# Optimization experiments

Hardware: AMD Instinct MI355X
Metric: run time of the kernel (lower is better)

Reference implementation:

```python
import jax, jax.numpy as jnp
import numpy as np

N = 100000

def _gcn_conv(x, W, b, row, col, norm, n_nodes):
    # x: [N, Fin], W: [Fin, Fout]; message = norm * (x W)[row], aggregated at col
    h = x @ W                                  # small GEMM
    msg = h[row] * norm[:, None]               # [E+N, Fout] gather (memory bound)
    out = jax.ops.segment_sum(msg, col, num_segments=n_nodes)
    return out + b

def _norm_coeffs(edge_index, n_nodes):
    # add self-loops, compute symmetric normalization deg^-1/2[row]*deg^-1/2[col]
    loops = jnp.arange(n_nodes, dtype=edge_index.dtype)
    row = jnp.concatenate([edge_index[0], loops])
    col = jnp.concatenate([edge_index[1], loops])
    deg = jax.ops.segment_sum(jnp.ones_like(col, dtype=jnp.float32), col,
                              num_segments=n_nodes)
    dinv = jnp.where(deg > 0, jax.lax.rsqrt(deg), 0.0)
    norm = dinv[row] * dinv[col]
    return row, col, norm

def setup_inputs() -> dict:
    key = jax.random.key(0)
    ks = jax.random.split(key, 4)
    x = jax.random.normal(ks[0], (N, 64), dtype=jnp.float32)
    edge_index = jax.random.randint(ks[1], (2, 1600000), 0, N, dtype=jnp.int64)
    W1 = jax.random.normal(ks[2], (64, 64), dtype=jnp.float32) / np.sqrt(64)
    b1 = jnp.zeros((64,), dtype=jnp.float32)
    W2 = jax.random.normal(ks[3], (64, 64), dtype=jnp.float32) / np.sqrt(64)
    b2 = jnp.zeros((64,), dtype=jnp.float32)
    return {"x": x, "edge_index": edge_index, "W1": W1, "b1": b1, "W2": W2, "b2": b2}

def reference(x, edge_index, W1, b1, W2, b2):
    row, col, norm = _norm_coeffs(edge_index, N)
    h = jax.nn.relu(_gcn_conv(x, W1, b1, row, col, norm, N))
    return _gcn_conv(h, W2, b2, row, col, norm, N)
```

## Files before the change

### kernel.cpp

```cpp
#include <hip/hip_runtime.h>


#define NPB 32
#define BSH 8
#define BSZ 256
#define PTILE 4096
#define CAP 6144
#define PADALLOW 3856
#define CROW (CAP + PADALLOW)

typedef __attribute__((ext_vector_type(8))) short bf16x8;
typedef __attribute__((ext_vector_type(4))) float f32x4;

__device__ __forceinline__ unsigned bf16_rne(float f) {
    unsigned b = __float_as_uint(f);
    return (b + 0x7fffu + ((b >> 16) & 1u)) >> 16;
}
__device__ __forceinline__ float bf16_lo(unsigned u) { return __uint_as_float(u << 16); }
__device__ __forceinline__ float bf16_hi(unsigned u) { return __uint_as_float(u & 0xffff0000u); }

__global__ __launch_bounds__(512) void k_count(const int* __restrict__ coli,
                                               int E, int N, int NB, int numTiles,
                                               int* __restrict__ tcnt) {
    __shared__ int hist[512];
    int t = threadIdx.x;
    int T = E + N;
    int tile = blockIdx.x;
    int tstart = tile * PTILE;
    int m = min(PTILE, T - tstart);
    for (int b = t; b < NB; b += 512) hist[b] = 0;
    __syncthreads();
    for (int i = t; i < m; i += 512) {
        int g = tstart + i;
        int c = (g < E) ? coli[g] : (g - E);
        atomicAdd(&hist[c >> BSH], 1);
    }
    __syncthreads();
    for (int b = t; b < NB; b += 512) tcnt[(size_t)tile * NB + b] = hist[b];
}

__global__ __launch_bounds__(512) void k_scan(int* __restrict__ tcnt,
                                              int* __restrict__ btot,
                                              int NB, int numTiles) {
    __shared__ int wsum[8];
    int b = blockIdx.x;
    int t = threadIdx.x;
    int lane = t & 63, wid = t >> 6;
    int base = 0;
    for (int c0 = 0; c0 < numTiles; c0 += 512) {
        int tt = c0 + t;
        int v = (tt < numTiles) ? tcnt[(size_t)tt * NB + b] : 0;
        int inc = v;
        #pragma unroll
        for (int d = 1; d < 64; d <<= 1) {
            int o = __shfl_up(inc, d);
            if (lane >= d) inc += o;
        }
        if (lane == 63) wsum[wid] = inc;
        __syncthreads();
        int woff = 0, ctot = 0;
        #pragma unroll
        for (int i = 0; i < 8; i++) {
            int s = wsum[i];
            if (i < wid) woff += s;
            ctot += s;
        }
        if (tt < numTiles) tcnt[(size_t)tt * NB + b] = b * CAP + base + woff + inc - v;
        base += ctot;
        __syncthreads();
    }
    if (t == 0) btot[b] = base;
}

__global__ __launch_bounds__(512) void k_scatter(const int* __restrict__ rowi,
                                                 const int* __restrict__ coli,
                                                 int E, int N, int NB, int numTiles,
                                                 const int* __restrict__ tcnt,
                                                 unsigned* __restrict__ pairs) {
    __shared__ int hist[512];
    __shared__ int lbase[512];
    __shared__ int gbase[512];
    __shared__ unsigned sorted[PTILE];
    __shared__ unsigned short sbkt[PTILE];
    __shared__ int wsum[8];
    int t = threadIdx.x;
    int T = E + N;
    int tile = blockIdx.x;
    int tstart = tile * PTILE;
    int m = min(PTILE, T - tstart);
    for (int b = t; b < NB; b += 512) {
        hist[b] = 0;
        gbase[b] = tcnt[(size_t)tile * NB + b];
    }
    __syncthreads();
    int c_reg[8];
    #pragma unroll
    for (int k = 0; k < 8; k++) {
        int i = t + k * 512;
        int c = 0;
        if (i < m) {
            int g = tstart + i;
            c = (g < E) ? coli[g] : (g - E);
            atomicAdd(&hist[c >> BSH], 1);
        }
        c_reg[k] = c;
    }
    __syncthreads();
    {
        int lane = t & 63, wid = t >> 6;
        int v = (t < NB) ? hist[t] : 0;
        int inc = v;
        #pragma unroll
        for (int d = 1; d < 64; d <<= 1) {
            int o = __shfl_up(inc, d);
            if (lane >= d) inc += o;
        }
        if (lane == 63) wsum[wid] = inc;
        __syncthreads();
        int woff = 0;
        for (int i = 0; i < wid; i++) woff += wsum[i];
        if (t < NB) lbase[t] = woff + inc - v;
        __syncthreads();
    }
    for (int b = t; b < NB; b += 512) hist[b] = 0;
    __syncthreads();
    #pragma unroll
    for (int k = 0; k < 8; k++) {
        int i = t + k * 512;
        if (i < m) {
            int g = tstart + i;
            int c = c_reg[k];
            int r = (g < E) ? rowi[g] : c;
            int b = c >> BSH;
            int lr = atomicAdd(&hist[b], 1);
            int pos = lbase[b] + lr;
            sorted[pos] = (unsigned)r | ((unsigned)(c & (BSZ - 1)) << 24);
            sbkt[pos] = (unsigned short)b;
        }
    }
    __syncthreads();
    for (int j = t; j < m; j += 512) {
        int b = sbkt[j];
        pairs[gbase[b] + (j - lbase[b])] = sorted[j];
    }
}

__global__ __launch_bounds__(1024) void k_bfill(const unsigned* __restrict__ pairs,
                                                const int* __restrict__ btot,
                                                int N,
                                                int* __restrict__ offsets,
                                                int* __restrict__ cnt,
                                                float* __restrict__ dinv,
                                                int* __restrict__ csrc) {
    __shared__ int scnt[BSZ];
    __shared__ int scur[BSZ];
    __shared__ int wsum[4];
    __shared__ int scsrc[CROW];
    int b = blockIdx.x;
    int t = threadIdx.x;
    int ebeg = b * CAP;
    int m = btot[b];
    int pbase = b * CROW;
    if (t < BSZ) scnt[t] = 0;
    __syncthreads();
    for (int i = t; i < m; i += 1024) {
        atomicAdd(&scnt[pairs[ebeg + i] >> 24], 1);
    }
    __syncthreads();
    int cval = 0, pc = 0, inc = 0;
    int lane = t & 63, wid = t >> 6;
    if (t < BSZ) {
        cval = scnt[t];
        pc = (cval + 15) & ~15;
        inc = pc;
        #pragma unroll
        for (int d = 1; d < 64; d <<= 1) {
            int o = __shfl_up(inc, d);
            if (lane >= d) inc += o;
        }
        if (lane == 63) wsum[wid] = inc;
    }
    __syncthreads();
    if (t < BSZ) {
        int woff = 0;
        for (int i = 0; i < wid; i++) woff += wsum[i];
        int offl = woff + inc - pc;
        int v = (b << BSH) + t;
        if (v < N) {
            offsets[v] = pbase + offl;
            cnt[v] = (cval + 1) & ~1;
            dinv[v] = rsqrtf((float)cval);
        }
        scur[t] = offl;
        for (int i = offl + cval; i < offl + pc; i++) scsrc[i] = N;
    }
    __syncthreads();
    for (int i = t; i < m; i += 1024) {
        unsigned pk = pairs[ebeg + i];
        int slot = atomicAdd(&scur[pk >> 24], 1);
        scsrc[slot] = (int)(pk & 0xFFFFFFu);
    }
    __syncthreads();
    int tot = wsum[0] + wsum[1] + wsum[2] + wsum[3];
    for (int j = t; j < tot; j += 1024) csrc[pbase + j] = scsrc[j];
}

template <bool BF16IN>
__global__ __launch_bounds__(256) void k_gemm(const void* __restrict__ Xv,
                                              const float* __restrict__ W,
                                              const float* __restrict__ dinv,
                                              unsigned* __restrict__ Hout,
                                              int N, int nSlabs, int slabStride) {
    __shared__ float SMEM[4224];
    int t = threadIdx.x;
    int lane = t & 63, w = t >> 6;
    int nn = lane & 15, kq = lane >> 4;

    for (int i = t; i < 1024; i += 256) ((float4*)SMEM)[i] = ((const float4*)W)[i];
    __syncthreads();
    bf16x8 Bf[2][4];
    #pragma unroll
    for (int kt = 0; kt < 2; kt++) {
        #pragma unroll
        for (int ct = 0; ct < 4; ct++) {
            union { bf16x8 v; unsigned short s[8]; } u;
            #pragma unroll
            for (int j = 0; j < 8; j++) {
                int k = kt * 32 + kq * 8 + j;
                u.s[j] = (unsigned short)bf16_rne(SMEM[k * 64 + ct * 16 + nn]);
            }
            Bf[kt][ct] = u.v;
        }
    }
    __syncthreads();

    float* outT = SMEM + w * 1056;

    for (int slab = blockIdx.x * 4 + w; slab < nSlabs; slab += slabStride) {
        int row0 = slab * 16;
        int rowA = min(row0 + nn, N - 1);
        bf16x8 A0, A1;
        if (BF16IN) {
            const uint4* X = (const uint4*)Xv;
            union { uint4 u; bf16x8 v; } a0, a1;
            a0.u = X[(size_t)rowA * 8 + kq];
            a1.u = X[(size_t)rowA * 8 + 4 + kq];
            A0 = a0.v; A1 = a1.v;
        } else {
            const float4* X = (const float4*)Xv;
            float4 f0 = X[(size_t)rowA * 16 + kq * 2];
            float4 f1 = X[(size_t)rowA * 16 + kq * 2 + 1];
            float4 f2 = X[(size_t)rowA * 16 + 8 + kq * 2];
            float4 f3 = X[(size_t)rowA * 16 + 8 + kq * 2 + 1];
            union { bf16x8 v; unsigned short s[8]; } a0, a1;
            a0.s[0] = (unsigned short)bf16_rne(f0.x); a0.s[1] = (unsigned short)bf16_rne(f0.y);
            a0.s[2] = (unsigned short)bf16_rne(f0.z); a0.s[3] = (unsigned short)bf16_rne(f0.w);
            a0.s[4] = (unsigned short)bf16_rne(f1.x); a0.s[5] = (unsigned short)bf16_rne(f1.y);
            a0.s[6] = (unsigned short)bf16_rne(f1.z); a0.s[7] = (unsigned short)bf16_rne(f1.w);
            a1.s[0] = (unsigned short)bf16_rne(f2.x); a1.s[1] = (unsigned short)bf16_rne(f2.y);
            a1.s[2] = (unsigned short)bf16_rne(f2.z); a1.s[3] = (unsigned short)bf16_rne(f2.w);
            a1.s[4] = (unsigned short)bf16_rne(f3.x); a1.s[5] = (unsigned short)bf16_rne(f3.y);
            a1.s[6] = (unsigned short)bf16_rne(f3.z); a1.s[7] = (unsigned short)bf16_rne(f3.w);
            A0 = a0.v; A1 = a1.v;
        }
        float dvm = dinv[rowA];

        f32x4 acc[4];
        #pragma unroll
        for (int ct = 0; ct < 4; ct++) acc[ct] = (f32x4){0.f, 0.f, 0.f, 0.f};
        #pragma unroll
        for (int ct = 0; ct < 4; ct++) {
            acc[ct] = __builtin_amdgcn_mfma_f32_16x16x32_bf16(A0, Bf[0][ct], acc[ct], 0, 0, 0);
            acc[ct] = __builtin_amdgcn_mfma_f32_16x16x32_bf16(A1, Bf[1][ct], acc[ct], 0, 0, 0);
        }

        #pragma unroll
        for (int reg = 0; reg < 4; reg++) {
            int r = kq * 4 + reg;
            float dv = __shfl(dvm, r);
            #pragma unroll
            for (int ct = 0; ct < 4; ct++) {
                outT[r * 66 + ct * 16 + nn] = acc[ct][reg] * dv;
            }
        }
        int rr = lane >> 2;
        int c0 = (lane & 3) * 16;
        int orow = row0 + rr;
        if (orow < N) {
            unsigned pk[8];
            #pragma unroll
            for (int i = 0; i < 8; i++) {
                float lo = outT[rr * 66 + c0 + 2 * i];
                float hi = outT[rr * 66 + c0 + 2 * i + 1];
                pk[i] = bf16_rne(lo) | (bf16_rne(hi) << 16);
            }
            uint4* dst = (uint4*)Hout + (size_t)orow * 8 + (lane & 3) * 2;
            dst[0] = make_uint4(pk[0], pk[1], pk[2], pk[3]);
            dst[1] = make_uint4(pk[4], pk[5], pk[6], pk[7]);
        } else if (orow == N) {
            uint4* dst = (uint4*)Hout + (size_t)N * 8 + (lane & 3) * 2;
            dst[0] = make_uint4(0, 0, 0, 0);
            dst[1] = make_uint4(0, 0, 0, 0);
        }
    }
}

template <bool RELU_BF16OUT>
__global__ __launch_bounds__(256) void k_agg(const uint4* __restrict__ H,
                                             const int* __restrict__ offsets,
                                             const int* __restrict__ cnt,
                                             const int* __restrict__ csrc,
                                             const float* __restrict__ dinv,
                                             const float* __restrict__ bias,
                                             void* __restrict__ outv, int N) {
    int t = threadIdx.x;
    int fl = t & 7;
    int v = blockIdx.x * NPB + (t >> 3);
    if (v >= N) return;
    int beg = offsets[v];
    int deg = cnt[v];
    const int2* cs2 = (const int2*)(csrc + beg);
    const char* hb = (const char*)H + ((unsigned)fl << 4);

    float a0 = 0.f, a1 = 0.f, a2 = 0.f, a3 = 0.f;
    float a4 = 0.f, a5 = 0.f, a6 = 0.f, a7 = 0.f;

#define ACC8(R) do {                                                        \
        uint4 dd = *(const uint4*)(hb + ((unsigned)(R) << 7));              \
        a0 += bf16_lo(dd.x); a1 += bf16_hi(dd.x);                           \
        a2 += bf16_lo(dd.y); a3 += bf16_hi(dd.y);                           \
        a4 += bf16_lo(dd.z); a5 += bf16_hi(dd.z);                           \
        a6 += bf16_lo(dd.w); a7 += bf16_hi(dd.w);                           \
    } while (0)

    int2 ss = cs2[0];
    for (int j = 2; j < deg; j += 2) {
        int2 nx = cs2[j >> 1];
        ACC8(ss.x);
        ACC8(ss.y);
        ss = nx;
    }
    ACC8(ss.x);
    ACC8(ss.y);
#undef ACC8

    float dv = dinv[v];
    const float4* b4 = (const float4*)bias;
    float4 bA = b4[fl * 2];
    float4 bB = b4[fl * 2 + 1];
    float r0 = fmaf(dv, a0, bA.x);
    float r1 = fmaf(dv, a1, bA.y);
    float r2 = fmaf(dv, a2, bA.z);
    float r3 = fmaf(dv, a3, bA.w);
    float r4 = fmaf(dv, a4, bB.x);
    float r5 = fmaf(dv, a5, bB.y);
    float r6 = fmaf(dv, a6, bB.z);
    float r7 = fmaf(dv, a7, bB.w);
    if (RELU_BF16OUT) {
        r0 = fmaxf(r0, 0.f); r1 = fmaxf(r1, 0.f);
        r2 = fmaxf(r2, 0.f); r3 = fmaxf(r3, 0.f);
        r4 = fmaxf(r4, 0.f); r5 = fmaxf(r5, 0.f);
        r6 = fmaxf(r6, 0.f); r7 = fmaxf(r7, 0.f);
        uint4 pk;
        pk.x = bf16_rne(r0) | (bf16_rne(r1) << 16);
        pk.y = bf16_rne(r2) | (bf16_rne(r3) << 16);
        pk.z = bf16_rne(r4) | (bf16_rne(r5) << 16);
        pk.w = bf16_rne(r6) | (bf16_rne(r7) << 16);
        ((uint4*)outv)[(size_t)v * 8 + fl] = pk;
    } else {
        float4* o = (float4*)outv + (size_t)v * 16 + fl * 2;
        o[0] = make_float4(r0, r1, r2, r3);
        o[1] = make_float4(r4, r5, r6, r7);
    }
}

extern "C" void kernel_launch(void* const* d_in, const int* in_sizes, int n_in,
                              void* d_out, int out_size, void* d_ws, size_t ws_size,
                              hipStream_t stream) {
    const float* x  = (const float*)d_in[0];
    const int*   ei = (const int*)d_in[1];
    const float* W1 = (const float*)d_in[2];
    const float* b1 = (const float*)d_in[3];
    const float* W2 = (const float*)d_in[4];
    const float* b2 = (const float*)d_in[5];
    float* out      = (float*)d_out;

    const int N = in_sizes[0] / 64;
    const int E = in_sizes[1] / 2;
    const int* row = ei;
    const int* col = ei + E;
    const int T = E + N;
    const int NB = (N + BSZ - 1) >> BSH;
    const int numTiles = (T + PTILE - 1) / PTILE;

    char* p = (char*)d_ws;
    auto alloc = [&](size_t bytes) { void* r = (void*)p; p += (bytes + 255) & ~(size_t)255; return r; };
    int*      tcnt    = (int*)alloc((size_t)NB * numTiles * 4);
    int*      btot    = (int*)alloc((size_t)(NB + 1) * 4);
    int*      offsets = (int*)alloc((size_t)N * 4);
    int*      cnt     = (int*)alloc((size_t)N * 4);
    float*    dinv    = (float*)alloc((size_t)N * 4);
    unsigned* pairs   = (unsigned*)alloc((size_t)NB * CAP * 4);
    int*      csrc    = (int*)alloc(((size_t)NB * CROW + 64) * 4);
    unsigned* hbuf    = (unsigned*)alloc((size_t)(N + 16) * 32 * 4);
    unsigned* abuf    = (unsigned*)alloc((size_t)(N + 16) * 32 * 4);

    k_count<<<numTiles, 512, 0, stream>>>(col, E, N, NB, numTiles, tcnt);
    k_scan<<<NB, 512, 0, stream>>>(tcnt, btot, NB, numTiles);
    k_scatter<<<numTiles, 512, 0, stream>>>(row, col, E, N, NB, numTiles, tcnt, pairs);
    k_bfill<<<NB, 1024, 0, stream>>>(pairs, btot, N, offsets, cnt, dinv, csrc);

    const int nSlabs = (N + 16) / 16;
    const int GEMM_BLOCKS = 1024;
    const int SLAB_STRIDE = GEMM_BLOCKS * 4;
    const int GB = (N + NPB - 1) / NPB;

    k_gemm<false><<<GEMM_BLOCKS, 256, 0, stream>>>(x, W1, dinv, hbuf, N, nSlabs, SLAB_STRIDE);
    k_agg<true><<<GB, 256, 0, stream>>>((const uint4*)hbuf, offsets, cnt, csrc, dinv, b1, abuf, N);
    k_gemm<true><<<GEMM_BLOCKS, 256, 0, stream>>>(abuf, W2, dinv, hbuf, N, nSlabs, SLAB_STRIDE);
    k_agg<false><<<GB, 256, 0, stream>>>((const uint4*)hbuf, offsets, cnt, csrc, dinv, b2, out, N);
}
```

Baseline: 198.0 us.

## Fuse scatter with first GEMM and merge tail stages behind grid barriers

```diff
diff --git a/kernel.cpp b/kernel.cpp
--- a/kernel.cpp
+++ b/kernel.cpp
@@ -1,13 +1,14 @@
 #include <hip/hip_runtime.h>
 
 
-#define NPB 32
 #define BSH 8
 #define BSZ 256
 #define PTILE 4096
 #define CAP 6144
 #define PADALLOW 3856
 #define CROW (CAP + PADALLOW)
+#define GEMMB 1024
+#define TGRID 768
 
 typedef __attribute__((ext_vector_type(8))) short bf16x8;
 typedef __attribute__((ext_vector_type(4))) float f32x4;
@@ -19,9 +20,21 @@
 __device__ __forceinline__ float bf16_lo(unsigned u) { return __uint_as_float(u << 16); }
 __device__ __forceinline__ float bf16_hi(unsigned u) { return __uint_as_float(u & 0xffff0000u); }
 
+__device__ __forceinline__ void gbar(int* bar, int idx, int nblk) {
+    __syncthreads();
+    if (threadIdx.x == 0) {
+        __threadfence();
+        __hip_atomic_fetch_add(&bar[idx], 1, __ATOMIC_ACQ_REL, __HIP_MEMORY_SCOPE_AGENT);
+        while (__hip_atomic_load(&bar[idx], __ATOMIC_ACQUIRE, __HIP_MEMORY_SCOPE_AGENT) < nblk)
+            __builtin_amdgcn_s_sleep(1);
+    }
+    __syncthreads();
+}
+
 __global__ __launch_bounds__(512) void k_count(const int* __restrict__ coli,
                                                int E, int N, int NB, int numTiles,
-                                               int* __restrict__ tcnt) {
+                                               int* __restrict__ tcnt,
+                                               int* __restrict__ deg) {
     __shared__ int hist[512];
     int t = threadIdx.x;
     int T = E + N;
@@ -34,9 +47,10 @@
         int g = tstart + i;
         int c = (g < E) ? coli[g] : (g - E);
         atomicAdd(&hist[c >> BSH], 1);
-    }
-    __syncthreads();
-    for (int b = t; b < NB; b += 512) tcnt[(size_t)tile * NB + b] = hist[b];
+        atomicAdd(&deg[c], 1);
+    }
+    __syncthreads();
+    for (int b = t; b < NB; b += 512) tcnt[tile * NB + b] = hist[b];
 }
 
 __global__ __launch_bounds__(512) void k_scan(int* __restrict__ tcnt,
@@ -49,7 +63,7 @@
     int base = 0;
     for (int c0 = 0; c0 < numTiles; c0 += 512) {
         int tt = c0 + t;
-        int v = (tt < numTiles) ? tcnt[(size_t)tt * NB + b] : 0;
+        int v = (tt < numTiles) ? tcnt[tt * NB + b] : 0;
         int inc = v;
         #pragma unroll
         for (int d = 1; d < 64; d <<= 1) {
@@ -65,158 +79,26 @@
             if (i < wid) woff += s;
             ctot += s;
         }
-        if (tt < numTiles) tcnt[(size_t)tt * NB + b] = b * CAP + base + woff + inc - v;
+        if (tt < numTiles) tcnt[tt * NB + b] = b * CAP + base + woff + inc - v;
         base += ctot;
         __syncthreads();
     }
     if (t == 0) btot[b] = base;
 }
 
-__global__ __launch_bounds__(512) void k_scatter(const int* __restrict__ rowi,
-                                                 const int* __restrict__ coli,
-                                                 int E, int N, int NB, int numTiles,
-                                                 const int* __restrict__ tcnt,
-                                                 unsigned* __restrict__ pairs) {
-    __shared__ int hist[512];
-    __shared__ int lbase[512];
-    __shared__ int gbase[512];
-    __shared__ unsigned sorted[PTILE];
-    __shared__ unsigned short sbkt[PTILE];
-    __shared__ int wsum[8];
-    int t = threadIdx.x;
-    int T = E + N;
-    int tile = blockIdx.x;
-    int tstart = tile * PTILE;
-    int m = min(PTILE, T - tstart);
-    for (int b = t; b < NB; b += 512) {
-        hist[b] = 0;
-        gbase[b] = tcnt[(size_t)tile * NB + b];
-    }
-    __syncthreads();
-    int c_reg[8];
-    #pragma unroll
-    for (int k = 0; k < 8; k++) {
-        int i = t + k * 512;
-        int c = 0;
-        if (i < m) {
-            int g = tstart + i;
-            c = (g < E) ? coli[g] : (g - E);
-            atomicAdd(&hist[c >> BSH], 1);
-        }
-        c_reg[k] = c;
-    }
-    __syncthreads();
-    {
-        int lane = t & 63, wid = t >> 6;
-        int v = (t < NB) ? hist[t] : 0;
-        int inc = v;
-        #pragma unroll
-        for (int d = 1; d < 64; d <<= 1) {
-            int o = __shfl_up(inc, d);
-            if (lane >= d) inc += o;
-        }
-        if (lane == 63) wsum[wid] = inc;
-        __syncthreads();
-        int woff = 0;
-        for (int i = 0; i < wid; i++) woff += wsum[i];
-        if (t < NB) lbase[t] = woff + inc - v;
-        __syncthreads();
-    }
-    for (int b = t; b < NB; b += 512) hist[b] = 0;
-    __syncthreads();
-    #pragma unroll
-    for (int k = 0; k < 8; k++) {
-        int i = t + k * 512;
-        if (i < m) {
-            int g = tstart + i;
-            int c = c_reg[k];
-            int r = (g < E) ? rowi[g] : c;
-            int b = c >> BSH;
-            int lr = atomicAdd(&hist[b], 1);
-            int pos = lbase[b] + lr;
-            sorted[pos] = (unsigned)r | ((unsigned)(c & (BSZ - 1)) << 24);
-            sbkt[pos] = (unsigned short)b;
-        }
-    }
-    __syncthreads();
-    for (int j = t; j < m; j += 512) {
-        int b = sbkt[j];
-        pairs[gbase[b] + (j - lbase[b])] = sorted[j];
-    }
-}
-
-__global__ __launch_bounds__(1024) void k_bfill(const unsigned* __restrict__ pairs,
-                                                const int* __restrict__ btot,
-                                                int N,
-                                                int* __restrict__ offsets,
-                                                int* __restrict__ cnt,
-                                                float* __restrict__ dinv,
-                                                int* __restrict__ csrc) {
-    __shared__ int scnt[BSZ];
-    __shared__ int scur[BSZ];
-    __shared__ int wsum[4];
-    __shared__ int scsrc[CROW];
-    int b = blockIdx.x;
-    int t = threadIdx.x;
-    int ebeg = b * CAP;
-    int m = btot[b];
-    int pbase = b * CROW;
-    if (t < BSZ) scnt[t] = 0;
-    __syncthreads();
-    for (int i = t; i < m; i += 1024) {
-        atomicAdd(&scnt[pairs[ebeg + i] >> 24], 1);
-    }
-    __syncthreads();
-    int cval = 0, pc = 0, inc = 0;
-    int lane = t & 63, wid = t >> 6;
-    if (t < BSZ) {
-        cval = scnt[t];
-        pc = (cval + 15) & ~15;
-        inc = pc;
-        #pragma unroll
-        for (int d = 1; d < 64; d <<= 1) {
-            int o = __shfl_up(inc, d);
-            if (lane >= d) inc += o;
-        }
-        if (lane == 63) wsum[wid] = inc;
-    }
-    __syncthreads();
-    if (t < BSZ) {
-        int woff = 0;
-        for (int i = 0; i < wid; i++) woff += wsum[i];
-        int offl = woff + inc - pc;
-        int v = (b << BSH) + t;
-        if (v < N) {
-            offsets[v] = pbase + offl;
-            cnt[v] = (cval + 1) & ~1;
-            dinv[v] = rsqrtf((float)cval);
-        }
-        scur[t] = offl;
-        for (int i = offl + cval; i < offl + pc; i++) scsrc[i] = N;
-    }
-    __syncthreads();
-    for (int i = t; i < m; i += 1024) {
-        unsigned pk = pairs[ebeg + i];
-        int slot = atomicAdd(&scur[pk >> 24], 1);
-        scsrc[slot] = (int)(pk & 0xFFFFFFu);
-    }
-    __syncthreads();
-    int tot = wsum[0] + wsum[1] + wsum[2] + wsum[3];
-    for (int j = t; j < tot; j += 1024) csrc[pbase + j] = scsrc[j];
-}
-
-template <bool BF16IN>
-__global__ __launch_bounds__(256) void k_gemm(const void* __restrict__ Xv,
-                                              const float* __restrict__ W,
-                                              const float* __restrict__ dinv,
-                                              unsigned* __restrict__ Hout,
-                                              int N, int nSlabs, int slabStride) {
-    __shared__ float SMEM[4224];
+template <bool BF16IN, int NT>
+__device__ __forceinline__ void gemm_body(const void* __restrict__ Xv,
+                                          const float* __restrict__ W,
+                                          const int* __restrict__ deg,
+                                          unsigned* __restrict__ Hout,
+                                          int N, int nSlabs, int blkLocal,
+                                          int nBlkLocal, float* SMEM) {
     int t = threadIdx.x;
     int lane = t & 63, w = t >> 6;
     int nn = lane & 15, kq = lane >> 4;
-
-    for (int i = t; i < 1024; i += 256) ((float4*)SMEM)[i] = ((const float4*)W)[i];
+    constexpr int NW = NT / 64;
+
+    for (int i = t; i < 1024; i += NT) ((float4*)SMEM)[i] = ((const float4*)W)[i];
     __syncthreads();
     bf16x8 Bf[2][4];
     #pragma unroll
@@ -236,7 +118,7 @@
 
     float* outT = SMEM + w * 1056;
 
-    for (int slab = blockIdx.x * 4 + w; slab < nSlabs; slab += slabStride) {
+    for (int slab = blkLocal * NW + w; slab < nSlabs; slab += nBlkLocal * NW) {
         int row0 = slab * 16;
         int rowA = min(row0 + nn, N - 1);
         bf16x8 A0, A1;
@@ -263,7 +145,7 @@
             a1.s[6] = (unsigned short)bf16_rne(f3.z); a1.s[7] = (unsigned short)bf16_rne(f3.w);
             A0 = a0.v; A1 = a1.v;
         }
-        float dvm = dinv[rowA];
+        float dvm = rsqrtf((float)deg[rowA]);
 
         f32x4 acc[4];
         #pragma unroll
@@ -305,25 +187,145 @@
     }
 }
 
-template <bool RELU_BF16OUT>
-__global__ __launch_bounds__(256) void k_agg(const uint4* __restrict__ H,
-                                             const int* __restrict__ offsets,
-                                             const int* __restrict__ cnt,
-                                             const int* __restrict__ csrc,
-                                             const float* __restrict__ dinv,
-                                             const float* __restrict__ bias,
-                                             void* __restrict__ outv, int N) {
-    int t = threadIdx.x;
-    int fl = t & 7;
-    int v = blockIdx.x * NPB + (t >> 3);
-    if (v >= N) return;
-    int beg = offsets[v];
-    int deg = cnt[v];
-    const int2* cs2 = (const int2*)(csrc + beg);
-    const char* hb = (const char*)H + ((unsigned)fl << 4);
-
-    float a0 = 0.f, a1 = 0.f, a2 = 0.f, a3 = 0.f;
-    float a4 = 0.f, a5 = 0.f, a6 = 0.f, a7 = 0.f;
+__global__ __launch_bounds__(512, 2) void k_scgm(const int* __restrict__ rowi,
+                                                 const int* __restrict__ coli,
+                                                 int E, int N, int NB, int numTiles,
+                                                 const int* __restrict__ tcnt,
+                                                 unsigned* __restrict__ pairs,
+                                                 const float* __restrict__ x,
+                                                 const float* __restrict__ W1,
+                                                 const int* __restrict__ deg,
+                                                 unsigned* __restrict__ hbuf,
+                                                 int nSlabs) {
+    __shared__ int SH[8448];
+    int bid = blockIdx.x;
+    int t = threadIdx.x;
+    if (bid >= numTiles) {
+        gemm_body<false, 512>(x, W1, deg, hbuf, N, nSlabs, bid - numTiles, GEMMB,
+                              (float*)SH);
+        return;
+    }
+    int* hist = SH;
+    int* lbase = SH + 512;
+    int* gbase = SH + 1024;
+    unsigned* sorted = (unsigned*)(SH + 1536);
+    unsigned short* sbkt = (unsigned short*)(SH + 5632);
+    int* wsum = SH + 7680;
+    int T = E + N;
+    int tstart = bid * PTILE;
+    int m = min(PTILE, T - tstart);
+    int lane = t & 63, wid = t >> 6;
+    for (int b = t; b < NB; b += 512) {
+        hist[b] = 0;
+        gbase[b] = tcnt[bid * NB + b];
+    }
+    __syncthreads();
+    int c_reg[8];
+    #pragma unroll
+    for (int k = 0; k < 8; k++) {
+        int i = t + k * 512;
+        int c = 0;
+        if (i < m) {
+            int g = tstart + i;
+            c = (g < E) ? coli[g] : (g - E);
+            atomicAdd(&hist[c >> BSH], 1);
+        }
+        c_reg[k] = c;
+    }
+    __syncthreads();
+    {
+        int v = (t < NB) ? hist[t] : 0;
+        int inc = v;
+        #pragma unroll
+        for (int d = 1; d < 64; d <<= 1) {
+            int o = __shfl_up(inc, d);
+            if (lane >= d) inc += o;
+        }
+        if (lane == 63) wsum[wid] = inc;
+        __syncthreads();
+        int woff = 0;
+        for (int i = 0; i < wid; i++) woff += wsum[i];
+        if (t < NB) lbase[t] = woff + inc - v;
+        __syncthreads();
+    }
+    for (int b = t; b < NB; b += 512) hist[b] = 0;
+    __syncthreads();
+    #pragma unroll
+    for (int k = 0; k < 8; k++) {
+        int i = t + k * 512;
+        if (i < m) {
+            int g = tstart + i;
+            int c = c_reg[k];
+            int r = (g < E) ? rowi[g] : c;
+            int b = c >> BSH;
+            int lr = atomicAdd(&hist[b], 1);
+            int pos = lbase[b] + lr;
+            sorted[pos] = (unsigned)r | ((unsigned)(c & (BSZ - 1)) << 24);
+            sbkt[pos] = (unsigned short)b;
+        }
+    }
+    __syncthreads();
+    for (int j = t; j < m; j += 512) {
+        int b = sbkt[j];
+        pairs[gbase[b] + (j - lbase[b])] = sorted[j];
+    }
+}
+
+__global__ __launch_bounds__(1024) void k_bfill(const unsigned* __restrict__ pairs,
+                                                const int* __restrict__ btot,
+                                                int N,
+                                                int* __restrict__ offsets,
+                                                int* __restrict__ cnt,
+                                                int* __restrict__ csrc) {
+    __shared__ int scnt[BSZ];
+    __shared__ int scur[BSZ];
+    __shared__ int wsum[4];
+    __shared__ int scsrc[CROW];
+    int b = blockIdx.x;
+    int t = threadIdx.x;
+    int ebeg = b * CAP;
+    int m = btot[b];
+    int pbase = b * CROW;
+    int lane = t & 63, wid = t >> 6;
+    if (t < BSZ) scnt[t] = 0;
+    __syncthreads();
+    for (int i = t; i < m; i += 1024) atomicAdd(&scnt[pairs[ebeg + i] >> 24], 1);
+    __syncthreads();
+    int cval = 0, pc = 0, inc = 0;
+    if (t < BSZ) {
+        cval = scnt[t];
+        pc = (cval + 15) & ~15;
+        inc = pc;
+        #pragma unroll
+        for (int d = 1; d < 64; d <<= 1) {
+            int o = __shfl_up(inc, d);
+            if (lane >= d) inc += o;
+        }
+        if (lane == 63) wsum[wid] = inc;
+    }
+    __syncthreads();
+    if (t < BSZ) {
+        int woff = 0;
+        for (int i = 0; i < wid; i++) woff += wsum[i];
+        int offl = woff + inc - pc;
+        int v = (b << BSH) + t;
+        if (v < N) {
+            offsets[v] = pbase + offl;
+            cnt[v] = (cval + 1) & ~1;
+        }
+        scur[t] = offl;
+        for (int i = offl + cval; i < offl + pc; i++) scsrc[i] = N;
+    }
+    __syncthreads();
+    for (int i = t; i < m; i += 1024) {
+        unsigned pk = pairs[ebeg + i];
+        int slot = atomicAdd(&scur[pk >> 24], 1);
+        scsrc[slot] = (int)(pk & 0xFFFFFFu);
+    }
+    __syncthreads();
+    int tot = wsum[0] + wsum[1] + wsum[2] + wsum[3];
+    for (int j = t; j < tot; j += 1024) csrc[pbase + j] = scsrc[j];
+}
 
 #define ACC8(R) do {                                                        \
         uint4 dd = *(const uint4*)(hb + ((unsigned)(R) << 7));              \
@@ -333,45 +335,83 @@
         a6 += bf16_lo(dd.w); a7 += bf16_hi(dd.w);                           \
     } while (0)
 
-    int2 ss = cs2[0];
-    for (int j = 2; j < deg; j += 2) {
-        int2 nx = cs2[j >> 1];
-        ACC8(ss.x);
-        ACC8(ss.y);
-        ss = nx;
-    }
-    ACC8(ss.x);
-    ACC8(ss.y);
-#undef ACC8
-
-    float dv = dinv[v];
+template <bool RELU_BF16OUT>
+__device__ __forceinline__ void agg_body(const uint4* __restrict__ H,
+                                         const int* __restrict__ offsets,
+                                         const int* __restrict__ cnt,
+                                         const int* __restrict__ csrc,
+                                         const int* __restrict__ deg,
+                                         const float* __restrict__ bias,
+                                         void* __restrict__ outv, int N,
+                                         int blk, int nblk) {
+    int t = threadIdx.x;
+    int fl = t & 7;
+    const char* hb = (const char*)H + ((unsigned)fl << 4);
     const float4* b4 = (const float4*)bias;
     float4 bA = b4[fl * 2];
     float4 bB = b4[fl * 2 + 1];
-    float r0 = fmaf(dv, a0, bA.x);
-    float r1 = fmaf(dv, a1, bA.y);
-    float r2 = fmaf(dv, a2, bA.z);
-    float r3 = fmaf(dv, a3, bA.w);
-    float r4 = fmaf(dv, a4, bB.x);
-    float r5 = fmaf(dv, a5, bB.y);
-    float r6 = fmaf(dv, a6, bB.z);
-    float r7 = fmaf(dv, a7, bB.w);
-    if (RELU_BF16OUT) {
-        r0 = fmaxf(r0, 0.f); r1 = fmaxf(r1, 0.f);
-        r2 = fmaxf(r2, 0.f); r3 = fmaxf(r3, 0.f);
-        r4 = fmaxf(r4, 0.f); r5 = fmaxf(r5, 0.f);
-        r6 = fmaxf(r6, 0.f); r7 = fmaxf(r7, 0.f);
-        uint4 pk;
-        pk.x = bf16_rne(r0) | (bf16_rne(r1) << 16);
-        pk.y = bf16_rne(r2) | (bf16_rne(r3) << 16);
-        pk.z = bf16_rne(r4) | (bf16_rne(r5) << 16);
-        pk.w = bf16_rne(r6) | (bf16_rne(r7) << 16);
-        ((uint4*)outv)[(size_t)v * 8 + fl] = pk;
-    } else {
-        float4* o = (float4*)outv + (size_t)v * 16 + fl * 2;
-        o[0] = make_float4(r0, r1, r2, r3);
-        o[1] = make_float4(r4, r5, r6, r7);
-    }
+    for (int v = blk * 32 + (t >> 3); v < N; v += nblk * 32) {
+        int beg = offsets[v];
+        int dg = cnt[v];
+        const int2* cs2 = (const int2*)(csrc + beg);
+        float a0 = 0.f, a1 = 0.f, a2 = 0.f, a3 = 0.f;
+        float a4 = 0.f, a5 = 0.f, a6 = 0.f, a7 = 0.f;
+        int2 ss = cs2[0];
+        for (int j = 2; j < dg; j += 2) {
+            int2 nx = cs2[j >> 1];
+            ACC8(ss.x);
+            ACC8(ss.y);
+            ss = nx;
+        }
+        ACC8(ss.x);
+        ACC8(ss.y);
+        float dv = rsqrtf((float)deg[v]);
+        float r0 = fmaf(dv, a0, bA.x);
+        float r1 = fmaf(dv, a1, bA.y);
+        float r2 = fmaf(dv, a2, bA.z);
+        float r3 = fmaf(dv, a3, bA.w);
+        float r4 = fmaf(dv, a4, bB.x);
+        float r5 = fmaf(dv, a5, bB.y);
+        float r6 = fmaf(dv, a6, bB.z);
+        float r7 = fmaf(dv, a7, bB.w);
+        if (RELU_BF16OUT) {
+            r0 = fmaxf(r0, 0.f); r1 = fmaxf(r1, 0.f);
+            r2 = fmaxf(r2, 0.f); r3 = fmaxf(r3, 0.f);
+            r4 = fmaxf(r4, 0.f); r5 = fmaxf(r5, 0.f);
+            r6 = fmaxf(r6, 0.f); r7 = fmaxf(r7, 0.f);
+            uint4 pk;
+            pk.x = bf16_rne(r0) | (bf16_rne(r1) << 16);
+            pk.y = bf16_rne(r2) | (bf16_rne(r3) << 16);
+            pk.z = bf16_rne(r4) | (bf16_rne(r5) << 16);
+            pk.w = bf16_rne(r6) | (bf16_rne(r7) << 16);
+            ((uint4*)outv)[(size_t)v * 8 + fl] = pk;
+        } else {
+            float4* o = (float4*)outv + (size_t)v * 16 + fl * 2;
+            o[0] = make_float4(r0, r1, r2, r3);
+            o[1] = make_float4(r4, r5, r6, r7);
+        }
+    }
+}
+
+__global__ __launch_bounds__(256, 4) void k_tail(const int* __restrict__ offsets,
+                                                 const int* __restrict__ cnt,
+                                                 const int* __restrict__ csrc,
+                                                 const int* __restrict__ deg,
+                                                 const float* __restrict__ b1,
+                                                 const float* __restrict__ W2,
+                                                 const float* __restrict__ b2,
+                                                 unsigned* hbuf, unsigned* abuf,
+                                                 float* __restrict__ out,
+                                                 int N, int nSlabs, int* bar) {
+    __shared__ float SMEM[4224];
+    int bid = blockIdx.x;
+    agg_body<true>((const uint4*)hbuf, offsets, cnt, csrc, deg, b1, abuf, N,
+                   bid, TGRID);
+    gbar(bar, 0, TGRID);
+    gemm_body<true, 256>(abuf, W2, deg, hbuf, N, nSlabs, bid, TGRID, SMEM);
+    gbar(bar, 1, TGRID);
+    agg_body<false>((const uint4*)hbuf, offsets, cnt, csrc, deg, b2, out, N,
+                    bid, TGRID);
 }
 
 extern "C" void kernel_launch(void* const* d_in, const int* in_sizes, int n_in,
@@ -395,28 +435,27 @@
 
     char* p = (char*)d_ws;
     auto alloc = [&](size_t bytes) { void* r = (void*)p; p += (bytes + 255) & ~(size_t)255; return r; };
+    int*      barDeg  = (int*)alloc((size_t)(16 + N) * 4);
+    int*      bar     = barDeg;
+    int*      deg     = barDeg + 16;
     int*      tcnt    = (int*)alloc((size_t)NB * numTiles * 4);
     int*      btot    = (int*)alloc((size_t)(NB + 1) * 4);
     int*      offsets = (int*)alloc((size_t)N * 4);
     int*      cnt     = (int*)alloc((size_t)N * 4);
-    float*    dinv    = (float*)alloc((size_t)N * 4);
     unsigned* pairs   = (unsigned*)alloc((size_t)NB * CAP * 4);
     int*      csrc    = (int*)alloc(((size_t)NB * CROW + 64) * 4);
     unsigned* hbuf    = (unsigned*)alloc((size_t)(N + 16) * 32 * 4);
     unsigned* abuf    = (unsigned*)alloc((size_t)(N + 16) * 32 * 4);
 
-    k_count<<<numTiles, 512, 0, stream>>>(col, E, N, NB, numTiles, tcnt);
+    const int nSlabs = (N + 16) / 16;
+
+    hipMemsetAsync(barDeg, 0, (size_t)(16 + N) * 4, stream);
+    k_count<<<numTiles, 512, 0, stream>>>(col, E, N, NB, numTiles, tcnt, deg);
     k_scan<<<NB, 512, 0, stream>>>(tcnt, btot, NB, numTiles);
-    k_scatter<<<numTiles, 512, 0, stream>>>(row, col, E, N, NB, numTiles, tcnt, pairs);
-    k_bfill<<<NB, 1024, 0, stream>>>(pairs, btot, N, offsets, cnt, dinv, csrc);
-
-    const int nSlabs = (N + 16) / 16;
-    const int GEMM_BLOCKS = 1024;
-    const int SLAB_STRIDE = GEMM_BLOCKS * 4;
-    const int GB = (N + NPB - 1) / NPB;
-
-    k_gemm<false><<<GEMM_BLOCKS, 256, 0, stream>>>(x, W1, dinv, hbuf, N, nSlabs, SLAB_STRIDE);
-    k_agg<true><<<GB, 256, 0, stream>>>((const uint4*)hbuf, offsets, cnt, csrc, dinv, b1, abuf, N);
-    k_gemm<true><<<GEMM_BLOCKS, 256, 0, stream>>>(abuf, W2, dinv, hbuf, N, nSlabs, SLAB_STRIDE);
-    k_agg<false><<<GB, 256, 0, stream>>>((const uint4*)hbuf, offsets, cnt, csrc, dinv, b2, out, N);
-}
+    k_scgm<<<numTiles + GEMMB, 512, 0, stream>>>(row, col, E, N, NB, numTiles,
+                                                 tcnt, pairs, x, W1, deg, hbuf,
+                                                 nSlabs);
+    k_bfill<<<NB, 1024, 0, stream>>>(pairs, btot, N, offsets, cnt, csrc);
+    k_tail<<<TGRID, 256, 0, stream>>>(offsets, cnt, csrc, deg, b1, W2, b2,
+                                      hbuf, abuf, out, N, nSlabs, bar);
+}
```

Measured after the change: 496.6 us. +150.9%, slower.

## Sort nodes by degree within each bucket to balance aggregation wavefronts

Applied to the files above, without the earlier changes.

```diff
diff --git a/kernel.cpp b/kernel.cpp
--- a/kernel.cpp
+++ b/kernel.cpp
@@ -88,6 +88,7 @@
     int tile = blockIdx.x;
     int tstart = tile * PTILE;
     int m = min(PTILE, T - tstart);
+    int lane = t & 63, wid = t >> 6;
     for (int b = t; b < NB; b += 512) {
         hist[b] = 0;
         gbase[b] = tcnt[(size_t)tile * NB + b];
@@ -107,7 +108,6 @@
     }
     __syncthreads();
     {
-        int lane = t & 63, wid = t >> 6;
         int v = (t < NB) ? hist[t] : 0;
         int inc = v;
         #pragma unroll
@@ -151,24 +151,28 @@
                                                 int* __restrict__ offsets,
                                                 int* __restrict__ cnt,
                                                 float* __restrict__ dinv,
-                                                int* __restrict__ csrc) {
+                                                int* __restrict__ csrc,
+                                                int* __restrict__ perm) {
     __shared__ int scnt[BSZ];
     __shared__ int scur[BSZ];
     __shared__ int wsum[4];
+    __shared__ int sbin[256];
+    __shared__ int wsum2[4];
     __shared__ int scsrc[CROW];
     int b = blockIdx.x;
     int t = threadIdx.x;
     int ebeg = b * CAP;
     int m = btot[b];
     int pbase = b * CROW;
-    if (t < BSZ) scnt[t] = 0;
-    __syncthreads();
-    for (int i = t; i < m; i += 1024) {
-        atomicAdd(&scnt[pairs[ebeg + i] >> 24], 1);
-    }
+    int lane = t & 63, wid = t >> 6;
+    if (t < BSZ) { scnt[t] = 0; sbin[t] = 0; }
+    __syncthreads();
+    for (int i = t; i < m; i += 1024) atomicAdd(&scnt[pairs[ebeg + i] >> 24], 1);
     __syncthreads();
     int cval = 0, pc = 0, inc = 0;
-    int lane = t & 63, wid = t >> 6;
+    int v = (b << BSH) + t;
+    bool v_ok = (t < BSZ) && (v < N);
+    int key = 0;
     if (t < BSZ) {
         cval = scnt[t];
         pc = (cval + 15) & ~15;
@@ -179,14 +183,32 @@
             if (lane >= d) inc += o;
         }
         if (lane == 63) wsum[wid] = inc;
-    }
-    __syncthreads();
+        key = min(cval, 255);
+    }
+    if (v_ok) atomicAdd(&sbin[key], 1);
+    __syncthreads();
+    int bv = 0, binc = 0;
+    if (t < 256) {
+        bv = sbin[t];
+        binc = bv;
+        #pragma unroll
+        for (int d = 1; d < 64; d <<= 1) {
+            int o = __shfl_up(binc, d);
+            if (lane >= d) binc += o;
+        }
+        if (lane == 63) wsum2[wid] = binc;
+    }
+    __syncthreads();
+    if (t < 256) {
+        int woff2 = 0;
+        for (int i = 0; i < wid; i++) woff2 += wsum2[i];
+        sbin[t] = woff2 + binc - bv;
+    }
     if (t < BSZ) {
         int woff = 0;
         for (int i = 0; i < wid; i++) woff += wsum[i];
         int offl = woff + inc - pc;
-        int v = (b << BSH) + t;
-        if (v < N) {
+        if (v_ok) {
             offsets[v] = pbase + offl;
             cnt[v] = (cval + 1) & ~1;
             dinv[v] = rsqrtf((float)cval);
@@ -195,6 +217,10 @@
         for (int i = offl + cval; i < offl + pc; i++) scsrc[i] = N;
     }
     __syncthreads();
+    if (v_ok) {
+        int slot = atomicAdd(&sbin[key], 1);
+        perm[(b << BSH) + slot] = v;
+    }
     for (int i = t; i < m; i += 1024) {
         unsigned pk = pairs[ebeg + i];
         int slot = atomicAdd(&scur[pk >> 24], 1);
@@ -312,11 +338,13 @@
                                              const int* __restrict__ csrc,
                                              const float* __restrict__ dinv,
                                              const float* __restrict__ bias,
+                                             const int* __restrict__ perm,
                                              void* __restrict__ outv, int N) {
     int t = threadIdx.x;
     int fl = t & 7;
-    int v = blockIdx.x * NPB + (t >> 3);
-    if (v >= N) return;
+    int idx = blockIdx.x * NPB + (t >> 3);
+    if (idx >= N) return;
+    int v = perm[idx];
     int beg = offsets[v];
     int deg = cnt[v];
     const int2* cs2 = (const int2*)(csrc + beg);
@@ -400,6 +428,7 @@
     int*      offsets = (int*)alloc((size_t)N * 4);
     int*      cnt     = (int*)alloc((size_t)N * 4);
     float*    dinv    = (float*)alloc((size_t)N * 4);
+    int*      perm    = (int*)alloc((size_t)(NB << BSH) * 4);
     unsigned* pairs   = (unsigned*)alloc((size_t)NB * CAP * 4);
     int*      csrc    = (int*)alloc(((size_t)NB * CROW + 64) * 4);
     unsigned* hbuf    = (unsigned*)alloc((size_t)(N + 16) * 32 * 4);
@@ -408,7 +437,7 @@
     k_count<<<numTiles, 512, 0, stream>>>(col, E, N, NB, numTiles, tcnt);
     k_scan<<<NB, 512, 0, stream>>>(tcnt, btot, NB, numTiles);
     k_scatter<<<numTiles, 512, 0, stream>>>(row, col, E, N, NB, numTiles, tcnt, pairs);
-    k_bfill<<<NB, 1024, 0, stream>>>(pairs, btot, N, offsets, cnt, dinv, csrc);
+    k_bfill<<<NB, 1024, 0, stream>>>(pairs, btot, N, offsets, cnt, dinv, csrc, perm);
 
     const int nSlabs = (N + 16) / 16;
     const int GEMM_BLOCKS = 1024;
@@ -416,7 +445,7 @@
     const int GB = (N + NPB - 1) / NPB;
 
     k_gemm<false><<<GEMM_BLOCKS, 256, 0, stream>>>(x, W1, dinv, hbuf, N, nSlabs, SLAB_STRIDE);
-    k_agg<true><<<GB, 256, 0, stream>>>((const uint4*)hbuf, offsets, cnt, csrc, dinv, b1, abuf, N);
+    k_agg<true><<<GB, 256, 0, stream>>>((const uint4*)hbuf, offsets, cnt, csrc, dinv, b1, perm, abuf, N);
     k_gemm<true><<<GEMM_BLOCKS, 256, 0, stream>>>(abuf, W2, dinv, hbuf, N, nSlabs, SLAB_STRIDE);
-    k_agg<false><<<GB, 256, 0, stream>>>((const uint4*)hbuf, offsets, cnt, csrc, dinv, b2, out, N);
-}
+    k_agg<false><<<GB, 256, 0, stream>>>((const uint4*)hbuf, offsets, cnt, csrc, dinv, b2, perm, out, N);
+}
```

Result: slower. 218.5 us (+10.4%).
